# Kernel optimization log

Hardware: AMD Instinct MI355X
Metric: run time of the kernel (lower is better)

## Reference

```python
import jax, jax.numpy as jnp
import numpy as np

N_CELLS = 8192
IN_DIM = 512
HID_DIM = 1024
OUT_DIM = 512
ENG_DIM = 128  # hardcoded MLP width in BenchMind
N_FACTIONS = 8
SYNC = 0.15
DEBATE = 0.15


def setup_inputs() -> dict:
    key = jax.random.key(0)
    ks = iter(jax.random.split(key, 40))

    def rn(shape, s=1.0):
        return jax.random.normal(next(ks), shape, dtype=jnp.float32) * s

    def lin(out_d, in_d):
        s = 1.0 / np.sqrt(in_d)
        return rn((out_d, in_d), s), rn((out_d,), s)

    a_W1, a_b1 = lin(ENG_DIM, IN_DIM + HID_DIM)
    a_W2, a_b2 = lin(OUT_DIM, ENG_DIM)
    g_W1, g_b1 = lin(ENG_DIM, IN_DIM + HID_DIM)
    g_W2, g_b2 = lin(OUT_DIM, ENG_DIM)
    gru_Wih, gru_bih = lin(3 * HID_DIM, OUT_DIM + 1)
    gru_Whh, gru_bhh = lin(3 * HID_DIM, HID_DIM)
    proj_W, proj_b = lin(HID_DIM, 2 * HID_DIM)
    head_W, head_b = lin(IN_DIM, OUT_DIM)

    psi = rn((N_CELLS, HID_DIM), 0.1)
    psi = psi / (jnp.linalg.norm(psi, axis=-1, keepdims=True) + 1e-8)
    rho_diag = psi ** 2
    rho_offdiag = rn((N_CELLS, HID_DIM), 0.1)
    hiddens = rn((N_CELLS, HID_DIM), 0.1)
    noise_diag = rn((N_CELLS, HID_DIM))
    noise_off = rn((N_CELLS, HID_DIM))
    x = rn((1, IN_DIM))
    gamma = jnp.float32(0.1)

    return dict(x=x, rho_diag=rho_diag, rho_offdiag=rho_offdiag, hiddens=hiddens,
                gamma=gamma, proj_W=proj_W, proj_b=proj_b,
                a_W1=a_W1, a_b1=a_b1, a_W2=a_W2, a_b2=a_b2,
                g_W1=g_W1, g_b1=g_b1, g_W2=g_W2, g_b2=g_b2,
                gru_Wih=gru_Wih, gru_bih=gru_bih, gru_Whh=gru_Whh, gru_bhh=gru_bhh,
                head_W=head_W, head_b=head_b,
                noise_diag=noise_diag, noise_off=noise_off, step=10)


def _process(x, rho_diag, rho_offdiag, hiddens, gamma, proj_W, proj_b,
             a_W1, a_b1, a_W2, a_b2, g_W1, g_b1, g_W2, g_b2,
             gru_Wih, gru_bih, gru_Whh, gru_bhh, head_W, head_b,
             noise_diag, noise_off, step):
    n = hiddens.shape[0]
    # --- decohere() --- (gamma used via .item() in torch -> non-differentiable)
    g = jax.lax.stop_gradient(jax.nn.sigmoid(gamma))
    rho_off = rho_offdiag * (1.0 - g)
    rho_d = jax.nn.softmax(rho_diag + noise_diag * g * 0.1, axis=-1)
    feat = jnp.concatenate([rho_d, jnp.abs(rho_off)], axis=-1)        # [N, 2H]
    inj = feat @ proj_W.T + proj_b                                     # [N, H]
    h = hiddens + jax.lax.stop_gradient(inj) * 0.1

    # --- batched BenchMind over all cells (torch loops cells one-by-one) ---
    xb = jnp.broadcast_to(x, (n, x.shape[-1]))
    comb = jnp.concatenate([xb, h], axis=-1)                           # [N, I+H]
    a = jax.nn.relu(comb @ a_W1.T + a_b1) @ a_W2.T + a_b2              # [N, O]
    gg = jax.nn.relu(comb @ g_W1.T + g_b1) @ g_W2.T + g_b2             # [N, O]
    out = a - gg
    tension = jnp.mean(out ** 2, axis=-1, keepdims=True)               # [N, 1]

    # GRUCell (torch gate order: r, z, n); inputs are detached in torch
    mem_in = jax.lax.stop_gradient(jnp.concatenate([out, tension], axis=-1))
    gi = mem_in @ gru_Wih.T + gru_bih                                  # [N, 3H]
    gh = h @ gru_Whh.T + gru_bhh                                       # [N, 3H]
    i_r, i_z, i_n = jnp.split(gi, 3, axis=-1)
    h_r, h_z, h_n = jnp.split(gh, 3, axis=-1)
    r = jax.nn.sigmoid(i_r + h_r)
    z = jax.nn.sigmoid(i_z + h_z)
    nn_ = jnp.tanh(i_n + r * h_n)
    new_h = jax.lax.stop_gradient((1.0 - z) * nn_ + z * h)             # .detach() in torch

    # --- faction_sync_debate ---
    nf = min(N_FACTIONS, n // 2)
    fs = n // nf
    hb = new_h[: nf * fs].reshape(nf, fs, -1)
    hb = (1.0 - SYNC) * hb + SYNC * hb.mean(axis=1, keepdims=True)
    if step > 5:
        glob = hb.mean(axis=1).mean(axis=0)                            # [H]
        dc = max(1, fs // 4)
        hb = hb.at[:, :dc].set((1.0 - DEBATE) * hb[:, :dc] + DEBATE * glob)
    new_h = hb.reshape(nf * fs, -1)

    # --- tension-weighted mixture (weights built from .item()s -> no grad) ---
    w = jax.nn.softmax(jax.lax.stop_gradient(tension[:, 0]))           # [N]
    combined = (w[:, None] * out).sum(axis=0, keepdims=True)           # [1, O]
    pred = combined @ head_W.T + head_b                                # [1, I]
    return pred, new_h


def reference(x, rho_diag, rho_offdiag, hiddens, gamma, proj_W, proj_b,
              a_W1, a_b1, a_W2, a_b2, g_W1, g_b1, g_W2, g_b2,
              gru_Wih, gru_bih, gru_Whh, gru_bhh, head_W, head_b,
              noise_diag, noise_off, step):
    return _process(x, rho_diag, rho_offdiag, hiddens, gamma, proj_W, proj_b,
                    a_W1, a_b1, a_W2, a_b2, g_W1, g_b1, g_W2, g_b2,
                    gru_Wih, gru_bih, gru_Whh, gru_bhh, head_W, head_b,
                    noise_diag, noise_off, step)
```

## Files before the change

kernel.cpp:

```cpp
#include <hip/hip_runtime.h>
#include <math.h>

#define NC 8192
#define ID 512
#define HD 1024
#define OD 512
#define ED 128
#define NF 8
#define FS (NC/NF)
#define DC (FS/4)

typedef __bf16 bf16x8 __attribute__((ext_vector_type(8)));
typedef float  f32x4  __attribute__((ext_vector_type(4)));

__device__ __forceinline__ float sigmf(float x){ return 1.0f/(1.0f+__expf(-x)); }

__device__ __forceinline__ unsigned short f2bf(float f){
  union { float f; unsigned u; } v; v.f = f;
  unsigned r = v.u + 0x7FFFu + ((v.u >> 16) & 1u);
  return (unsigned short)(r >> 16);
}
__device__ __forceinline__ float bf2f(unsigned short b){
  union { unsigned u; float f; } v; v.u = ((unsigned)b) << 16;
  return v.f;
}
__device__ __forceinline__ void gload16(const void* g, void* l){
  __builtin_amdgcn_global_load_lds(
      (const __attribute__((address_space(1))) unsigned int*)g,
      (__attribute__((address_space(3))) unsigned int*)l, 16, 0, 0);
}

__global__ __launch_bounds__(256) void k_conv(
    const float* __restrict__ src, unsigned short* __restrict__ dst,
    int rows, int cols, int sld, int sofs, int dld, float scale)
{
  int i = blockIdx.x*256 + threadIdx.x;
  int total = rows*cols/4;
  if (i >= total) return;
  int r = (i*4)/cols, c = (i*4)%cols;
  const float* s = src + (size_t)r*sld + sofs + c;
  unsigned long long pack = 0;
  for (int q=0;q<4;q++)
    pack |= (unsigned long long)f2bf(s[q]*scale) << (16*q);
  *reinterpret_cast<unsigned long long*>(&dst[(size_t)r*dld + c]) = pack;
}

__global__ __launch_bounds__(256) void k_convgru(
    const float* __restrict__ Wih, const float* __restrict__ Whh,
    unsigned short* __restrict__ dst)
{
  int i = blockIdx.x*256 + threadIdx.x;
  const int total = 3*1024*1536/4;
  if (i >= total) return;
  int row = (i*4)/1536, c = (i*4)%1536;
  unsigned long long pack = 0;
  if (c < 512){
    const float* s = Wih + (size_t)row*(OD+1) + c;
    for (int q=0;q<4;q++) pack |= (unsigned long long)f2bf(s[q]) << (16*q);
  } else {
    const float* s = Whh + (size_t)row*HD + (c-512);
    for (int q=0;q<4;q++) pack |= (unsigned long long)f2bf(s[q]) << (16*q);
  }
  *reinterpret_cast<unsigned long long*>(&dst[(size_t)row*1536 + c]) = pack;
}

__global__ __launch_bounds__(256) void k_feat(
    const float* __restrict__ rho_diag, const float* __restrict__ noise_diag,
    const float* __restrict__ rho_off,  const float* __restrict__ gamma,
    unsigned short* __restrict__ featb)
{
  int row = blockIdx.x;
  int t = threadIdx.x;
  float g = 1.0f/(1.0f+__expf(-gamma[0]));
  const float* rd = rho_diag  + (size_t)row*HD;
  const float* nd = noise_diag+ (size_t)row*HD;
  const float* ro = rho_off   + (size_t)row*HD;
  unsigned short* f0 = featb + (size_t)row*(2*HD);

  float v[4];
  float mx = -1e30f;
  for (int i=0;i<4;i++){ int j=t+i*256; v[i] = rd[j] + nd[j]*g*0.1f; mx = fmaxf(mx, v[i]); }
  __shared__ float red[256];
  red[t]=mx; __syncthreads();
  for(int s=128;s>0;s>>=1){ if(t<s) red[t]=fmaxf(red[t],red[t+s]); __syncthreads(); }
  mx = red[0]; __syncthreads();
  float sm=0.0f;
  for(int i=0;i<4;i++){ v[i]=__expf(v[i]-mx); sm+=v[i]; }
  red[t]=sm; __syncthreads();
  for(int s=128;s>0;s>>=1){ if(t<s) red[t]+=red[t+s]; __syncthreads(); }
  float inv = 1.0f/red[0];
  float om_g = 1.0f - g;
  for(int i=0;i<4;i++){
    int j=t+i*256;
    f0[j]     = f2bf(v[i]*inv);
    f0[HD+j]  = f2bf(fabsf(ro[j])*om_g);
  }
}

template<int MODE>
__global__ __launch_bounds__(256) void k_mgemm(
    const unsigned short* __restrict__ A, int lda,
    const unsigned short* __restrict__ W,
    int K, int N,
    float* __restrict__ Cf, int ldcf,
    unsigned short* __restrict__ Cb, int ldcb,
    const float* __restrict__ e0, const float* __restrict__ e1)
{
  __shared__ __attribute__((aligned(16))) unsigned short Asb[128*32];
  __shared__ __attribute__((aligned(16))) unsigned short Bsb[128*32];
  const int t = threadIdx.x;
  const int lane = t & 63, wid = t >> 6;
  const int wr = wid >> 1, wc = wid & 1;

  const int nwg = gridDim.x*gridDim.y;
  const int bid = blockIdx.y*gridDim.x + blockIdx.x;
  const int swz = (bid & 7)*(nwg >> 3) + (bid >> 3);
  const int m0 = (swz / gridDim.x) * 128, n0 = (swz % gridDim.x) * 128;

  const int srow = lane >> 2;
  const int skch = (lane & 3) * 8;
  const int fr = lane & 15, fk = (lane >> 4) * 8;

  f32x4 acc[4][4] = {};
  for (int k0 = 0; k0 < K; k0 += 32) {
    for (int q = 0; q < 2; ++q) {
      int r = wid*32 + q*16 + srow;
      gload16(A + (size_t)(m0 + r)*lda + k0 + skch, &Asb[(wid*32 + q*16)*32]);
      gload16(W + (size_t)(n0 + r)*K   + k0 + skch, &Bsb[(wid*32 + q*16)*32]);
    }
    __syncthreads();
    bf16x8 af[4], bfr[4];
    for (int i = 0; i < 4; ++i)
      af[i]  = *reinterpret_cast<const bf16x8*>(&Asb[(wr*64 + i*16 + fr)*32 + fk]);
    for (int j = 0; j < 4; ++j)
      bfr[j] = *reinterpret_cast<const bf16x8*>(&Bsb[(wc*64 + j*16 + fr)*32 + fk]);
    for (int i = 0; i < 4; ++i)
      for (int j = 0; j < 4; ++j)
        acc[i][j] = __builtin_amdgcn_mfma_f32_16x16x32_bf16(af[i], bfr[j], acc[i][j], 0, 0, 0);
    __syncthreads();
  }
  const int cr = (lane >> 4) * 4;
  const int cc = lane & 15;
  for (int i = 0; i < 4; ++i){
    for (int j = 0; j < 4; ++j){
      for (int r = 0; r < 4; ++r){
        int m = m0 + wr*64 + i*16 + cr + r;
        int n = n0 + wc*64 + j*16 + cc;
        float v = acc[i][j][r];
        if (MODE == 0)      v = e0[(size_t)m*N + n] + 0.1f*(v + e1[n]);
        else if (MODE == 1) v = fmaxf(v + e0[n], 0.0f);
        else if (MODE == 2) v = v + e0[n];
        if (MODE == 2) Cf[(size_t)m*ldcf + n] = v;
        Cb[(size_t)m*ldcb + n] = f2bf(v);
      }
    }
  }
}

__global__ __launch_bounds__(256) void k_gru_mega(
    const unsigned short* __restrict__ Acat,
    const unsigned short* __restrict__ Wg,
    const float* __restrict__ bih, const float* __restrict__ bhh,
    const float* __restrict__ tens, const float* __restrict__ wlast,
    float* __restrict__ newh)
{
  __shared__ __attribute__((aligned(16))) unsigned short As[64*32];
  __shared__ __attribute__((aligned(16))) unsigned short Rs[64*32];
  __shared__ __attribute__((aligned(16))) unsigned short Zs[64*32];
  __shared__ __attribute__((aligned(16))) unsigned short Ns[64*32];
  const int t = threadIdx.x;
  const int lane = t & 63, wid = t >> 6;
  const int wr = wid >> 1, wc = wid & 1;

  const int nwg = gridDim.x*gridDim.y;
  const int bid = blockIdx.y*gridDim.x + blockIdx.x;
  const int swz = (bid & 7)*(nwg >> 3) + (bid >> 3);
  const int m0 = (swz >> 4) * 64, n0 = (swz & 15) * 64;

  const int srow = lane >> 2;
  const int skch = (lane & 3) * 8;
  const int fr = lane & 15, fk = (lane >> 4) * 8;

  const unsigned short* sbase;
  unsigned short* lbase;
  if      (wid == 0){ sbase = Acat + (size_t)m0*1536;              lbase = As; }
  else if (wid == 1){ sbase = Wg   + (size_t)n0*1536;              lbase = Rs; }
  else if (wid == 2){ sbase = Wg + (size_t)(HD + n0)*1536;         lbase = Zs; }
  else              { sbase = Wg + (size_t)(2*HD + n0)*1536;       lbase = Ns; }

  f32x4 acc_r[2][2] = {}, acc_z[2][2] = {}, acc_na[2][2] = {}, acc_nb[2][2] = {};

  for (int k0 = 0; k0 < 1536; k0 += 32) {
    for (int q = 0; q < 4; ++q)
      gload16(sbase + (size_t)(q*16 + srow)*1536 + k0 + skch, &lbase[(q*16)*32]);
    __syncthreads();
    bf16x8 af[2], br[2], bz[2], bn[2];
    for (int i = 0; i < 2; ++i)
      af[i] = *reinterpret_cast<const bf16x8*>(&As[(wr*32 + i*16 + fr)*32 + fk]);
    for (int j = 0; j < 2; ++j){
      br[j] = *reinterpret_cast<const bf16x8*>(&Rs[(wc*32 + j*16 + fr)*32 + fk]);
      bz[j] = *reinterpret_cast<const bf16x8*>(&Zs[(wc*32 + j*16 + fr)*32 + fk]);
      bn[j] = *reinterpret_cast<const bf16x8*>(&Ns[(wc*32 + j*16 + fr)*32 + fk]);
    }
    if (k0 < 512){
      for (int i = 0; i < 2; ++i)
        for (int j = 0; j < 2; ++j){
          acc_r [i][j] = __builtin_amdgcn_mfma_f32_16x16x32_bf16(af[i], br[j], acc_r [i][j], 0,0,0);
          acc_z [i][j] = __builtin_amdgcn_mfma_f32_16x16x32_bf16(af[i], bz[j], acc_z [i][j], 0,0,0);
          acc_na[i][j] = __builtin_amdgcn_mfma_f32_16x16x32_bf16(af[i], bn[j], acc_na[i][j], 0,0,0);
        }
    } else {
      for (int i = 0; i < 2; ++i)
        for (int j = 0; j < 2; ++j){
          acc_r [i][j] = __builtin_amdgcn_mfma_f32_16x16x32_bf16(af[i], br[j], acc_r [i][j], 0,0,0);
          acc_z [i][j] = __builtin_amdgcn_mfma_f32_16x16x32_bf16(af[i], bz[j], acc_z [i][j], 0,0,0);
          acc_nb[i][j] = __builtin_amdgcn_mfma_f32_16x16x32_bf16(af[i], bn[j], acc_nb[i][j], 0,0,0);
        }
    }
    __syncthreads();
  }

  const int cr = (lane >> 4) * 4;
  const int cc = lane & 15;
  for (int i = 0; i < 2; ++i){
    for (int r = 0; r < 4; ++r){
      int m = m0 + wr*32 + i*16 + cr + r;
      float tm = tens[m];
      for (int j = 0; j < 2; ++j){
        int n = n0 + wc*32 + j*16 + cc;
        float sr  = acc_r [i][j][r] + bih[n]      + tm*wlast[n]      + bhh[n];
        float sz  = acc_z [i][j][r] + bih[HD+n]   + tm*wlast[HD+n]   + bhh[HD+n];
        float sni = acc_na[i][j][r] + bih[2*HD+n] + tm*wlast[2*HD+n];
        float snh = acc_nb[i][j][r] + bhh[2*HD+n];
        float rg = sigmf(sr);
        float zg = sigmf(sz);
        float nn = tanhf(sni + rg*snh);
        float hv = bf2f(Acat[(size_t)m*1536 + 512 + n]);
        newh[(size_t)m*HD + n] = (1.0f - zg)*nn + zg*hv;
      }
    }
  }
}

__global__ __launch_bounds__(128) void k_xpart(
    const float* __restrict__ x,
    const float* __restrict__ aW1, const float* __restrict__ ab1,
    const float* __restrict__ gW1, const float* __restrict__ gb1,
    const float* __restrict__ Wih,
    const float* __restrict__ ab2, const float* __restrict__ gb2,
    float* __restrict__ xcat, float* __restrict__ wlast, float* __restrict__ b2diff)
{
  int t = threadIdx.x;
  if (blockIdx.x == 2){
    for (int n=t; n<3*HD; n+=128) wlast[n] = Wih[(size_t)n*(OD+1) + OD];
    for (int n=t; n<OD;   n+=128) b2diff[n] = ab2[n] - gb2[n];
    return;
  }
  const float* W = blockIdx.x ? gW1 : aW1;
  const float* b = blockIdx.x ? gb1 : ab1;
  float s = b[t];
  const float* wr = W + (size_t)t*(ID+HD);
  for (int k=0;k<ID;k++) s += x[k]*wr[k];
  xcat[blockIdx.x*ED + t] = s;
}

__global__ __launch_bounds__(256) void k_tension(
    const float* __restrict__ outp, float* __restrict__ tens)
{
  int m = blockIdx.x, t = threadIdx.x;
  float s = 0.0f;
  for (int j=t;j<OD;j+=256){ float v = outp[(size_t)m*OD + j]; s += v*v; }
  __shared__ float red[256];
  red[t]=s; __syncthreads();
  for(int k=128;k>0;k>>=1){ if(t<k) red[t]+=red[t+k]; __syncthreads(); }
  if (t==0) tens[m] = red[0] * (1.0f/OD);
}

__global__ __launch_bounds__(256) void k_fmean(
    const float* __restrict__ newh, float* __restrict__ fmean)
{
  int f = blockIdx.x;
  int j = blockIdx.y*256 + threadIdx.x;
  const float* base = newh + (size_t)f*FS*HD + j;
  float s = 0.0f;
  for (int c=0;c<FS;c++) s += base[(size_t)c*HD];
  fmean[f*HD + j] = s * (1.0f/FS);
}

__global__ __launch_bounds__(256) void k_sync(
    float* __restrict__ newh, const float* __restrict__ fmean,
    const int* __restrict__ step)
{
  size_t idx = (size_t)blockIdx.x*256 + threadIdx.x;
  int cell = (int)(idx / HD);
  int j    = (int)(idx % HD);
  int f = cell / FS, c = cell % FS;
  float v = newh[idx];
  v = 0.85f*v + 0.15f*fmean[f*HD + j];
  if (step[0] > 5 && c < DC){
    float glob = 0.0f;
    for (int ff=0; ff<NF; ff++) glob += fmean[ff*HD + j];
    glob *= (1.0f/NF);
    v = 0.85f*v + 0.15f*glob;
  }
  newh[idx] = v;
}

__global__ __launch_bounds__(1024) void k_wstats(
    const float* __restrict__ tens, float* __restrict__ stats)
{
  int t = threadIdx.x;
  float mx = -1e30f;
  for (int i=t;i<NC;i+=1024) mx = fmaxf(mx, tens[i]);
  __shared__ float red[1024];
  red[t]=mx; __syncthreads();
  for(int s=512;s>0;s>>=1){ if(t<s) red[t]=fmaxf(red[t],red[t+s]); __syncthreads(); }
  mx = red[0]; __syncthreads();
  float sm=0.0f;
  for (int i=t;i<NC;i+=1024) sm += __expf(tens[i]-mx);
  red[t]=sm; __syncthreads();
  for(int s=512;s>0;s>>=1){ if(t<s) red[t]+=red[t+s]; __syncthreads(); }
  if (t==0){ stats[0]=mx; stats[1]=red[0]; }
}

__global__ __launch_bounds__(256) void k_wnorm(
    const float* __restrict__ tens, const float* __restrict__ stats,
    float* __restrict__ w)
{
  int m = blockIdx.x*256 + threadIdx.x;
  w[m] = __expf(tens[m]-stats[0]) * (1.0f/stats[1]);
}

__global__ __launch_bounds__(256) void k_comb1(
    const float* __restrict__ outp, const float* __restrict__ w,
    float* __restrict__ partial)
{
  int b = blockIdx.x, t = threadIdx.x;
  float a0 = 0.0f, a1 = 0.0f;
  for (int m = 0; m < 128; ++m){
    int row = b*128 + m;
    float wm = w[row];
    const float* r = outp + (size_t)row*OD;
    a0 += wm * r[t];
    a1 += wm * r[t+256];
  }
  partial[(size_t)b*OD + t]       = a0;
  partial[(size_t)b*OD + t + 256] = a1;
}

__global__ __launch_bounds__(256) void k_comb2(
    const float* __restrict__ partial, float* __restrict__ comb)
{
  int n = blockIdx.x*256 + threadIdx.x;
  float s = 0.0f;
  for (int b = 0; b < 64; ++b) s += partial[(size_t)b*OD + n];
  comb[n] = s;
}

__global__ __launch_bounds__(128) void k_pred(
    const float* __restrict__ comb, const float* __restrict__ headW,
    const float* __restrict__ headb, float* __restrict__ pred)
{
  int i = blockIdx.x, t = threadIdx.x;
  float s = 0.0f;
  const float* wr = headW + (size_t)i*OD;
  for (int k=t;k<OD;k+=128) s += comb[k]*wr[k];
  __shared__ float red[128];
  red[t]=s; __syncthreads();
  for (int sx=64;sx>0;sx>>=1){ if(t<sx) red[t]+=red[t+sx]; __syncthreads(); }
  if (t==0) pred[i] = red[0] + headb[i];
}

extern "C" void kernel_launch(void* const* d_in, const int* in_sizes, int n_in,
                              void* d_out, int out_size, void* d_ws, size_t ws_size,
                              hipStream_t stream)
{
  const float* x        = (const float*)d_in[0];
  const float* rho_diag = (const float*)d_in[1];
  const float* rho_off  = (const float*)d_in[2];
  const float* hiddens  = (const float*)d_in[3];
  const float* gamma    = (const float*)d_in[4];
  const float* proj_W   = (const float*)d_in[5];
  const float* proj_b   = (const float*)d_in[6];
  const float* a_W1     = (const float*)d_in[7];
  const float* a_b1     = (const float*)d_in[8];
  const float* a_W2     = (const float*)d_in[9];
  const float* a_b2     = (const float*)d_in[10];
  const float* g_W1     = (const float*)d_in[11];
  const float* g_b1     = (const float*)d_in[12];
  const float* g_W2     = (const float*)d_in[13];
  const float* g_b2     = (const float*)d_in[14];
  const float* gru_Wih  = (const float*)d_in[15];
  const float* gru_bih  = (const float*)d_in[16];
  const float* gru_Whh  = (const float*)d_in[17];
  const float* gru_bhh  = (const float*)d_in[18];
  const float* head_W   = (const float*)d_in[19];
  const float* head_b   = (const float*)d_in[20];
  const float* noise_d  = (const float*)d_in[21];
  const int*   step     = (const int*)d_in[23];

  float* pred = (float*)d_out;
  float* newh = (float*)d_out + ID;

  char* ws = (char*)d_ws;
  const size_t MB = 1024*1024;
  unsigned short* Acat   = (unsigned short*)(ws + 0);
  unsigned short* featb  = (unsigned short*)(ws + 24*MB);
  float*          outp_f = (float*)(ws + 56*MB);
  unsigned short* eag    = (unsigned short*)(ws + 72*MB);
  unsigned short* wProj  = (unsigned short*)(ws + 76*MB);
  unsigned short* wGru   = (unsigned short*)(ws + 80*MB);
  unsigned short* wEng   = (unsigned short*)(ws + 89*MB);
  unsigned short* wW2    = (unsigned short*)(ws + 89*MB + 512*1024);
  char* sm = ws + 90*MB;
  float* tens    = (float*)(sm + 0);
  float* xcat    = (float*)(sm + 64*1024);
  float* wlast   = (float*)(sm + 128*1024);
  float* b2diff  = (float*)(sm + 160*1024);
  float* fmean   = (float*)(sm + 192*1024);
  float* stats   = (float*)(sm + 256*1024);
  float* wts     = (float*)(sm + 320*1024);
  float* partial = (float*)(sm + 384*1024);
  float* comb    = (float*)(sm + 576*1024);

  dim3 blk(256);
  #define CONVGRID(n) dim3(((n)/4 + 255)/256)

  k_conv<<<CONVGRID(1024*2048), blk, 0, stream>>>(proj_W, wProj, 1024, 2048, 2048, 0, 2048, 1.0f);
  k_convgru<<<dim3(3*1024*1536/4/256), blk, 0, stream>>>(gru_Wih, gru_Whh, wGru);
  k_conv<<<CONVGRID(128*1024), blk, 0, stream>>>(a_W1, wEng,            128, 1024, ID+HD, ID, 1024, 1.0f);
  k_conv<<<CONVGRID(128*1024), blk, 0, stream>>>(g_W1, wEng + 128*1024, 128, 1024, ID+HD, ID, 1024, 1.0f);
  k_conv<<<CONVGRID(512*128),  blk, 0, stream>>>(a_W2, wW2,       512, 128, 128, 0, 256,  1.0f);
  k_conv<<<CONVGRID(512*128),  blk, 0, stream>>>(g_W2, wW2 + 128, 512, 128, 128, 0, 256, -1.0f);

  k_feat<<<dim3(NC), blk, 0, stream>>>(rho_diag, noise_d, rho_off, gamma, featb);
  k_xpart<<<dim3(3), dim3(128), 0, stream>>>(x, a_W1, a_b1, g_W1, g_b1, gru_Wih,
                                             a_b2, g_b2, xcat, wlast, b2diff);

  k_mgemm<0><<<dim3(HD/128, NC/128), blk, 0, stream>>>(
      featb, 2*HD, wProj, 2*HD, HD, nullptr, 0, Acat + 512, 1536, hiddens, proj_b);
  k_mgemm<1><<<dim3(256/128, NC/128), blk, 0, stream>>>(
      Acat + 512, 1536, wEng, HD, 256, nullptr, 0, eag, 256, xcat, nullptr);
  k_mgemm<2><<<dim3(OD/128, NC/128), blk, 0, stream>>>(
      eag, 256, wW2, 256, OD, outp_f, OD, Acat, 1536, b2diff, nullptr);
  k_tension<<<dim3(NC), blk, 0, stream>>>(outp_f, tens);
  k_gru_mega<<<dim3(HD/64, NC/64), blk, 0, stream>>>(
      Acat, wGru, gru_bih, gru_bhh, tens, wlast, newh);
  k_fmean<<<dim3(NF, HD/256), blk, 0, stream>>>(newh, fmean);
  k_sync<<<dim3((NC*HD)/256), blk, 0, stream>>>(newh, fmean, step);
  k_wstats<<<dim3(1), dim3(1024), 0, stream>>>(tens, stats);
  k_wnorm<<<dim3(NC/256), blk, 0, stream>>>(tens, stats, wts);
  k_comb1<<<dim3(64), blk, 0, stream>>>(outp_f, wts, partial);
  k_comb2<<<dim3(2), blk, 0, stream>>>(partial, comb);
  k_pred<<<dim3(ID), dim3(128), 0, stream>>>(comb, head_W, head_b, pred);
}
```

Before: 602.8 us.

## Double-buffer LDS tiles in GEMM and GRU kernels, reorder block mapping

Both the generic MFMA GEMM and the fused GRU kernel now use two LDS buffers per operand, so the next K-slice is loaded while the current one is consumed, which removes one barrier per iteration. The workgroup-to-tile mapping is also changed to walk along M first within each N column, so neighbouring blocks reuse the same weight tile in cache. LDS use doubles, which may lower occupancy. Correctness relies on the gload16 async copy having completed by the single barrier at the end of each iteration.

```diff
diff --git a/kernel.cpp b/kernel.cpp
--- a/kernel.cpp
+++ b/kernel.cpp
@@ -106,8 +106,8 @@
     unsigned short* __restrict__ Cb, int ldcb,
     const float* __restrict__ e0, const float* __restrict__ e1)
 {
-  __shared__ __attribute__((aligned(16))) unsigned short Asb[128*32];
-  __shared__ __attribute__((aligned(16))) unsigned short Bsb[128*32];
+  __shared__ __attribute__((aligned(16))) unsigned short Asb[2][128*32];
+  __shared__ __attribute__((aligned(16))) unsigned short Bsb[2][128*32];
   const int t = threadIdx.x;
   const int lane = t & 63, wid = t >> 6;
   const int wr = wid >> 1, wc = wid & 1;
@@ -115,30 +115,45 @@
   const int nwg = gridDim.x*gridDim.y;
   const int bid = blockIdx.y*gridDim.x + blockIdx.x;
   const int swz = (bid & 7)*(nwg >> 3) + (bid >> 3);
-  const int m0 = (swz / gridDim.x) * 128, n0 = (swz % gridDim.x) * 128;
+  const int n0 = (swz / gridDim.y) * 128, m0 = (swz % gridDim.y) * 128;
 
   const int srow = lane >> 2;
   const int skch = (lane & 3) * 8;
   const int fr = lane & 15, fk = (lane >> 4) * 8;
 
+  const int nk = K >> 5;
   f32x4 acc[4][4] = {};
-  for (int k0 = 0; k0 < K; k0 += 32) {
+
+  {
     for (int q = 0; q < 2; ++q) {
       int r = wid*32 + q*16 + srow;
-      gload16(A + (size_t)(m0 + r)*lda + k0 + skch, &Asb[(wid*32 + q*16)*32]);
-      gload16(W + (size_t)(n0 + r)*K   + k0 + skch, &Bsb[(wid*32 + q*16)*32]);
-    }
-    __syncthreads();
+      gload16(A + (size_t)(m0 + r)*lda + skch, &Asb[0][(wid*32 + q*16)*32]);
+      gload16(W + (size_t)(n0 + r)*K   + skch, &Bsb[0][(wid*32 + q*16)*32]);
+    }
+  }
+  __syncthreads();
+
+  for (int kk = 0; kk < nk; ++kk) {
+    const int buf = kk & 1;
+    if (kk + 1 < nk) {
+      const int k0 = (kk + 1) << 5;
+      for (int q = 0; q < 2; ++q) {
+        int r = wid*32 + q*16 + srow;
+        gload16(A + (size_t)(m0 + r)*lda + k0 + skch, &Asb[buf^1][(wid*32 + q*16)*32]);
+        gload16(W + (size_t)(n0 + r)*K   + k0 + skch, &Bsb[buf^1][(wid*32 + q*16)*32]);
+      }
+    }
     bf16x8 af[4], bfr[4];
     for (int i = 0; i < 4; ++i)
-      af[i]  = *reinterpret_cast<const bf16x8*>(&Asb[(wr*64 + i*16 + fr)*32 + fk]);
+      af[i]  = *reinterpret_cast<const bf16x8*>(&Asb[buf][(wr*64 + i*16 + fr)*32 + fk]);
     for (int j = 0; j < 4; ++j)
-      bfr[j] = *reinterpret_cast<const bf16x8*>(&Bsb[(wc*64 + j*16 + fr)*32 + fk]);
+      bfr[j] = *reinterpret_cast<const bf16x8*>(&Bsb[buf][(wc*64 + j*16 + fr)*32 + fk]);
     for (int i = 0; i < 4; ++i)
       for (int j = 0; j < 4; ++j)
         acc[i][j] = __builtin_amdgcn_mfma_f32_16x16x32_bf16(af[i], bfr[j], acc[i][j], 0, 0, 0);
     __syncthreads();
   }
+
   const int cr = (lane >> 4) * 4;
   const int cc = lane & 15;
   for (int i = 0; i < 4; ++i){
@@ -164,10 +179,10 @@
     const float* __restrict__ tens, const float* __restrict__ wlast,
     float* __restrict__ newh)
 {
-  __shared__ __attribute__((aligned(16))) unsigned short As[64*32];
-  __shared__ __attribute__((aligned(16))) unsigned short Rs[64*32];
-  __shared__ __attribute__((aligned(16))) unsigned short Zs[64*32];
-  __shared__ __attribute__((aligned(16))) unsigned short Ns[64*32];
+  __shared__ __attribute__((aligned(16))) unsigned short As[2][64*32];
+  __shared__ __attribute__((aligned(16))) unsigned short Rs[2][64*32];
+  __shared__ __attribute__((aligned(16))) unsigned short Zs[2][64*32];
+  __shared__ __attribute__((aligned(16))) unsigned short Ns[2][64*32];
   const int t = threadIdx.x;
   const int lane = t & 63, wid = t >> 6;
   const int wr = wid >> 1, wc = wid & 1;
@@ -175,42 +190,58 @@
   const int nwg = gridDim.x*gridDim.y;
   const int bid = blockIdx.y*gridDim.x + blockIdx.x;
   const int swz = (bid & 7)*(nwg >> 3) + (bid >> 3);
-  const int m0 = (swz >> 4) * 64, n0 = (swz & 15) * 64;
+  const int n0 = (swz / gridDim.y) * 64, m0 = (swz % gridDim.y) * 64;
 
   const int srow = lane >> 2;
   const int skch = (lane & 3) * 8;
   const int fr = lane & 15, fk = (lane >> 4) * 8;
 
   const unsigned short* sbase;
-  unsigned short* lbase;
-  if      (wid == 0){ sbase = Acat + (size_t)m0*1536;              lbase = As; }
-  else if (wid == 1){ sbase = Wg   + (size_t)n0*1536;              lbase = Rs; }
-  else if (wid == 2){ sbase = Wg + (size_t)(HD + n0)*1536;         lbase = Zs; }
-  else              { sbase = Wg + (size_t)(2*HD + n0)*1536;       lbase = Ns; }
+  unsigned short* lb0; unsigned short* lb1;
+  if      (wid == 0){ sbase = Acat + (size_t)m0*1536;          lb0 = As[0]; lb1 = As[1]; }
+  else if (wid == 1){ sbase = Wg   + (size_t)n0*1536;          lb0 = Rs[0]; lb1 = Rs[1]; }
+  else if (wid == 2){ sbase = Wg + (size_t)(HD   + n0)*1536;   lb0 = Zs[0]; lb1 = Zs[1]; }
+  else              { sbase = Wg + (size_t)(2*HD + n0)*1536;   lb0 = Ns[0]; lb1 = Ns[1]; }
 
   f32x4 acc_r[2][2] = {}, acc_z[2][2] = {}, acc_na[2][2] = {}, acc_nb[2][2] = {};
 
-  for (int k0 = 0; k0 < 1536; k0 += 32) {
-    for (int q = 0; q < 4; ++q)
-      gload16(sbase + (size_t)(q*16 + srow)*1536 + k0 + skch, &lbase[(q*16)*32]);
-    __syncthreads();
+  #pragma unroll
+  for (int q = 0; q < 4; ++q)
+    gload16(sbase + (size_t)(q*16 + srow)*1536 + skch, &lb0[(q*16)*32]);
+  __syncthreads();
+
+  for (int kk = 0; kk < 48; ++kk) {
+    const int buf = kk & 1;
+    if (kk < 47) {
+      const int k0 = (kk + 1) << 5;
+      unsigned short* lb = buf ? lb0 : lb1;
+      #pragma unroll
+      for (int q = 0; q < 4; ++q)
+        gload16(sbase + (size_t)(q*16 + srow)*1536 + k0 + skch, &lb[(q*16)*32]);
+    }
     bf16x8 af[2], br[2], bz[2], bn[2];
+    #pragma unroll
     for (int i = 0; i < 2; ++i)
-      af[i] = *reinterpret_cast<const bf16x8*>(&As[(wr*32 + i*16 + fr)*32 + fk]);
+      af[i] = *reinterpret_cast<const bf16x8*>(&As[buf][(wr*32 + i*16 + fr)*32 + fk]);
+    #pragma unroll
     for (int j = 0; j < 2; ++j){
-      br[j] = *reinterpret_cast<const bf16x8*>(&Rs[(wc*32 + j*16 + fr)*32 + fk]);
-      bz[j] = *reinterpret_cast<const bf16x8*>(&Zs[(wc*32 + j*16 + fr)*32 + fk]);
-      bn[j] = *reinterpret_cast<const bf16x8*>(&Ns[(wc*32 + j*16 + fr)*32 + fk]);
-    }
-    if (k0 < 512){
+      br[j] = *reinterpret_cast<const bf16x8*>(&Rs[buf][(wc*32 + j*16 + fr)*32 + fk]);
+      bz[j] = *reinterpret_cast<const bf16x8*>(&Zs[buf][(wc*32 + j*16 + fr)*32 + fk]);
+      bn[j] = *reinterpret_cast<const bf16x8*>(&Ns[buf][(wc*32 + j*16 + fr)*32 + fk]);
+    }
+    if (kk < 16){
+      #pragma unroll
       for (int i = 0; i < 2; ++i)
+        #pragma unroll
         for (int j = 0; j < 2; ++j){
           acc_r [i][j] = __builtin_amdgcn_mfma_f32_16x16x32_bf16(af[i], br[j], acc_r [i][j], 0,0,0);
           acc_z [i][j] = __builtin_amdgcn_mfma_f32_16x16x32_bf16(af[i], bz[j], acc_z [i][j], 0,0,0);
           acc_na[i][j] = __builtin_amdgcn_mfma_f32_16x16x32_bf16(af[i], bn[j], acc_na[i][j], 0,0,0);
         }
     } else {
+      #pragma unroll
       for (int i = 0; i < 2; ++i)
+        #pragma unroll
         for (int j = 0; j < 2; ++j){
           acc_r [i][j] = __builtin_amdgcn_mfma_f32_16x16x32_bf16(af[i], br[j], acc_r [i][j], 0,0,0);
           acc_z [i][j] = __builtin_amdgcn_mfma_f32_16x16x32_bf16(af[i], bz[j], acc_z [i][j], 0,0,0);
```

New measurement: 591.7 us. Within noise of the previous version (-1.8%).

## Triple-buffer GEMM LDS loads and merge weight-prep kernels into one launch

Applied to the files above, without the earlier changes.

Both MFMA GEMM kernels now use three LDS buffers, issuing global-to-LDS loads two k-steps ahead and waiting with explicit vmcnt counts before each barrier. This replaces the load-sync-compute-sync pattern so memory latency can overlap with the MFMA work. The mgemm tile order is changed to walk M-major within N columns. The six weight conversion kernels and the x-projection kernel are merged into a single k_prep launch to cut launch overhead. The cost is three times the LDS per block, which may lower occupancy.

```diff
diff --git a/kernel.cpp b/kernel.cpp
--- a/kernel.cpp
+++ b/kernel.cpp
@@ -29,39 +29,62 @@
       (const __attribute__((address_space(1))) unsigned int*)g,
       (__attribute__((address_space(3))) unsigned int*)l, 16, 0, 0);
 }
-
-__global__ __launch_bounds__(256) void k_conv(
-    const float* __restrict__ src, unsigned short* __restrict__ dst,
-    int rows, int cols, int sld, int sofs, int dld, float scale)
-{
-  int i = blockIdx.x*256 + threadIdx.x;
-  int total = rows*cols/4;
-  if (i >= total) return;
-  int r = (i*4)/cols, c = (i*4)%cols;
-  const float* s = src + (size_t)r*sld + sofs + c;
-  unsigned long long pack = 0;
-  for (int q=0;q<4;q++)
-    pack |= (unsigned long long)f2bf(s[q]*scale) << (16*q);
-  *reinterpret_cast<unsigned long long*>(&dst[(size_t)r*dld + c]) = pack;
-}
-
-__global__ __launch_bounds__(256) void k_convgru(
-    const float* __restrict__ Wih, const float* __restrict__ Whh,
-    unsigned short* __restrict__ dst)
-{
-  int i = blockIdx.x*256 + threadIdx.x;
-  const int total = 3*1024*1536/4;
-  if (i >= total) return;
-  int row = (i*4)/1536, c = (i*4)%1536;
-  unsigned long long pack = 0;
-  if (c < 512){
-    const float* s = Wih + (size_t)row*(OD+1) + c;
-    for (int q=0;q<4;q++) pack |= (unsigned long long)f2bf(s[q]) << (16*q);
+__device__ __forceinline__ void pack4(const float* s, unsigned short* d, float sc){
+  unsigned long long p = 0;
+  for (int q=0;q<4;q++) p |= (unsigned long long)f2bf(s[q]*sc) << (16*q);
+  *reinterpret_cast<unsigned long long*>(d) = p;
+}
+
+#define WAIT_VM4()  asm volatile("s_waitcnt vmcnt(4)" ::: "memory")
+#define WAIT_VM0()  asm volatile("s_waitcnt vmcnt(0)" ::: "memory")
+#define BARRIER()   do { __builtin_amdgcn_s_barrier(); asm volatile("" ::: "memory"); } while(0)
+
+__global__ __launch_bounds__(256) void k_prep(
+    const float* __restrict__ proj_W, const float* __restrict__ Wih,
+    const float* __restrict__ Whh,
+    const float* __restrict__ aW1, const float* __restrict__ gW1,
+    const float* __restrict__ aW2, const float* __restrict__ gW2,
+    const float* __restrict__ x,
+    const float* __restrict__ ab1, const float* __restrict__ gb1,
+    const float* __restrict__ ab2, const float* __restrict__ gb2,
+    unsigned short* __restrict__ wProj, unsigned short* __restrict__ wGru,
+    unsigned short* __restrict__ wEng,  unsigned short* __restrict__ wW2,
+    float* __restrict__ xcat, float* __restrict__ wlast,
+    float* __restrict__ b2diff)
+{
+  int b = blockIdx.x, t = threadIdx.x;
+  if (b < 2048){
+    int i = b*256 + t; int r = (i*4)>>11, c = (i*4)&2047;
+    pack4(proj_W + (size_t)r*2048 + c, wProj + (size_t)r*2048 + c, 1.0f);
+  } else if (b < 6656){
+    int i = (b-2048)*256 + t; int row = (i*4)/1536, c = (i*4)%1536;
+    const float* s = (c < 512) ? (Wih + (size_t)row*(OD+1) + c)
+                               : (Whh + (size_t)row*HD + (c-512));
+    pack4(s, wGru + (size_t)row*1536 + c, 1.0f);
+  } else if (b < 6784){
+    int i = (b-6656)*256 + t; int r = (i*4)>>10, c = (i*4)&1023;
+    pack4(aW1 + (size_t)r*(ID+HD) + ID + c, wEng + (size_t)r*1024 + c, 1.0f);
+  } else if (b < 6912){
+    int i = (b-6784)*256 + t; int r = (i*4)>>10, c = (i*4)&1023;
+    pack4(gW1 + (size_t)r*(ID+HD) + ID + c, wEng + 128*1024 + (size_t)r*1024 + c, 1.0f);
+  } else if (b < 6976){
+    int i = (b-6912)*256 + t; int r = (i*4)>>7, c = (i*4)&127;
+    pack4(aW2 + (size_t)r*128 + c, wW2 + (size_t)r*256 + c, 1.0f);
+  } else if (b < 7040){
+    int i = (b-6976)*256 + t; int r = (i*4)>>7, c = (i*4)&127;
+    pack4(gW2 + (size_t)r*128 + c, wW2 + (size_t)r*256 + 128 + c, -1.0f);
+  } else if (b == 7040){
+    const float* W  = (t < 128) ? aW1 : gW1;
+    const float* bb = (t < 128) ? ab1 : gb1;
+    int n = t & 127;
+    float s = bb[n];
+    const float* wr = W + (size_t)n*(ID+HD);
+    for (int k=0;k<ID;k++) s += x[k]*wr[k];
+    xcat[t] = s;
   } else {
-    const float* s = Whh + (size_t)row*HD + (c-512);
-    for (int q=0;q<4;q++) pack |= (unsigned long long)f2bf(s[q]) << (16*q);
-  }
-  *reinterpret_cast<unsigned long long*>(&dst[(size_t)row*1536 + c]) = pack;
+    for (int n=t; n<3*HD; n+=256) wlast[n] = Wih[(size_t)n*(OD+1) + OD];
+    for (int n=t; n<OD;   n+=256) b2diff[n] = ab2[n] - gb2[n];
+  }
 }
 
 __global__ __launch_bounds__(256) void k_feat(
@@ -106,8 +129,8 @@
     unsigned short* __restrict__ Cb, int ldcb,
     const float* __restrict__ e0, const float* __restrict__ e1)
 {
-  __shared__ __attribute__((aligned(16))) unsigned short Asb[128*32];
-  __shared__ __attribute__((aligned(16))) unsigned short Bsb[128*32];
+  __shared__ __attribute__((aligned(16))) unsigned short Asb[3][128*32];
+  __shared__ __attribute__((aligned(16))) unsigned short Bsb[3][128*32];
   const int t = threadIdx.x;
   const int lane = t & 63, wid = t >> 6;
   const int wr = wid >> 1, wc = wid & 1;
@@ -115,30 +138,51 @@
   const int nwg = gridDim.x*gridDim.y;
   const int bid = blockIdx.y*gridDim.x + blockIdx.x;
   const int swz = (bid & 7)*(nwg >> 3) + (bid >> 3);
-  const int m0 = (swz / gridDim.x) * 128, n0 = (swz % gridDim.x) * 128;
+  const int n0 = (swz / gridDim.y) * 128, m0 = (swz % gridDim.y) * 128;
 
   const int srow = lane >> 2;
   const int skch = (lane & 3) * 8;
   const int fr = lane & 15, fk = (lane >> 4) * 8;
 
+  const int nk = K >> 5;
   f32x4 acc[4][4] = {};
-  for (int k0 = 0; k0 < K; k0 += 32) {
+
+  auto STAGE = [&](int kc, int bf){
+    const int k0 = kc << 5;
     for (int q = 0; q < 2; ++q) {
       int r = wid*32 + q*16 + srow;
-      gload16(A + (size_t)(m0 + r)*lda + k0 + skch, &Asb[(wid*32 + q*16)*32]);
-      gload16(W + (size_t)(n0 + r)*K   + k0 + skch, &Bsb[(wid*32 + q*16)*32]);
-    }
-    __syncthreads();
+      gload16(A + (size_t)(m0 + r)*lda + k0 + skch, &Asb[bf][(wid*32 + q*16)*32]);
+      gload16(W + (size_t)(n0 + r)*K   + k0 + skch, &Bsb[bf][(wid*32 + q*16)*32]);
+    }
+  };
+
+  STAGE(0, 0);
+  if (nk > 1) { STAGE(1, 1); WAIT_VM4(); } else { WAIT_VM0(); }
+  BARRIER();
+
+  for (int kk = 0; kk < nk; ++kk) {
+    const int buf = kk % 3;
+    if (kk + 2 < nk) STAGE(kk + 2, (kk + 2) % 3);
+    const unsigned short* Ab = &Asb[buf][0];
+    const unsigned short* Bb = &Bsb[buf][0];
     bf16x8 af[4], bfr[4];
+    #pragma unroll
     for (int i = 0; i < 4; ++i)
-      af[i]  = *reinterpret_cast<const bf16x8*>(&Asb[(wr*64 + i*16 + fr)*32 + fk]);
+      af[i]  = *reinterpret_cast<const bf16x8*>(&Ab[(wr*64 + i*16 + fr)*32 + fk]);
+    #pragma unroll
     for (int j = 0; j < 4; ++j)
-      bfr[j] = *reinterpret_cast<const bf16x8*>(&Bsb[(wc*64 + j*16 + fr)*32 + fk]);
+      bfr[j] = *reinterpret_cast<const bf16x8*>(&Bb[(wc*64 + j*16 + fr)*32 + fk]);
+    #pragma unroll
     for (int i = 0; i < 4; ++i)
+      #pragma unroll
       for (int j = 0; j < 4; ++j)
         acc[i][j] = __builtin_amdgcn_mfma_f32_16x16x32_bf16(af[i], bfr[j], acc[i][j], 0, 0, 0);
-    __syncthreads();
-  }
+    if (kk + 1 < nk) {
+      if (kk + 2 < nk) WAIT_VM4(); else WAIT_VM0();
+      BARRIER();
+    }
+  }
+
   const int cr = (lane >> 4) * 4;
   const int cc = lane & 15;
   for (int i = 0; i < 4; ++i){
@@ -164,10 +208,10 @@
     const float* __restrict__ tens, const float* __restrict__ wlast,
     float* __restrict__ newh)
 {
-  __shared__ __attribute__((aligned(16))) unsigned short As[64*32];
-  __shared__ __attribute__((aligned(16))) unsigned short Rs[64*32];
-  __shared__ __attribute__((aligned(16))) unsigned short Zs[64*32];
-  __shared__ __attribute__((aligned(16))) unsigned short Ns[64*32];
+  __shared__ __attribute__((aligned(16))) unsigned short As[3][64*32];
+  __shared__ __attribute__((aligned(16))) unsigned short Rs[3][64*32];
+  __shared__ __attribute__((aligned(16))) unsigned short Zs[3][64*32];
+  __shared__ __attribute__((aligned(16))) unsigned short Ns[3][64*32];
   const int t = threadIdx.x;
   const int lane = t & 63, wid = t >> 6;
   const int wr = wid >> 1, wc = wid & 1;
@@ -182,42 +226,68 @@
   const int fr = lane & 15, fk = (lane >> 4) * 8;
 
   const unsigned short* sbase;
-  unsigned short* lbase;
-  if      (wid == 0){ sbase = Acat + (size_t)m0*1536;              lbase = As; }
-  else if (wid == 1){ sbase = Wg   + (size_t)n0*1536;              lbase = Rs; }
-  else if (wid == 2){ sbase = Wg + (size_t)(HD + n0)*1536;         lbase = Zs; }
-  else              { sbase = Wg + (size_t)(2*HD + n0)*1536;       lbase = Ns; }
+  unsigned short* lb;
+  if      (wid == 0){ sbase = Acat + (size_t)m0*1536;          lb = &As[0][0]; }
+  else if (wid == 1){ sbase = Wg   + (size_t)n0*1536;          lb = &Rs[0][0]; }
+  else if (wid == 2){ sbase = Wg + (size_t)(HD   + n0)*1536;   lb = &Zs[0][0]; }
+  else              { sbase = Wg + (size_t)(2*HD + n0)*1536;   lb = &Ns[0][0]; }
 
   f32x4 acc_r[2][2] = {}, acc_z[2][2] = {}, acc_na[2][2] = {}, acc_nb[2][2] = {};
 
-  for (int k0 = 0; k0 < 1536; k0 += 32) {
+  auto STAGE = [&](int kc, int bf){
+    const int k0 = kc << 5;
+    #pragma unroll
     for (int q = 0; q < 4; ++q)
-      gload16(sbase + (size_t)(q*16 + srow)*1536 + k0 + skch, &lbase[(q*16)*32]);
-    __syncthreads();
+      gload16(sbase + (size_t)(q*16 + srow)*1536 + k0 + skch,
+              lb + bf*(64*32) + (q*16)*32);
+  };
+
+  STAGE(0, 0);
+  STAGE(1, 1);
+  WAIT_VM4();
+  BARRIER();
+
+  const int nk = 48;
+  for (int kk = 0; kk < nk; ++kk) {
+    const int buf = kk % 3;
+    if (kk + 2 < nk) STAGE(kk + 2, (kk + 2) % 3);
+    const unsigned short* Ab = &As[0][0] + buf*(64*32);
+    const unsigned short* Rb = &Rs[0][0] + buf*(64*32);
+    const unsigned short* Zb = &Zs[0][0] + buf*(64*32);
+    const unsigned short* Nb = &Ns[0][0] + buf*(64*32);
     bf16x8 af[2], br[2], bz[2], bn[2];
+    #pragma unroll
     for (int i = 0; i < 2; ++i)
-      af[i] = *reinterpret_cast<const bf16x8*>(&As[(wr*32 + i*16 + fr)*32 + fk]);
+      af[i] = *reinterpret_cast<const bf16x8*>(&Ab[(wr*32 + i*16 + fr)*32 + fk]);
+    #pragma unroll
     for (int j = 0; j < 2; ++j){
-      br[j] = *reinterpret_cast<const bf16x8*>(&Rs[(wc*32 + j*16 + fr)*32 + fk]);
-      bz[j] = *reinterpret_cast<const bf16x8*>(&Zs[(wc*32 + j*16 + fr)*32 + fk]);
-      bn[j] = *reinterpret_cast<const bf16x8*>(&Ns[(wc*32 + j*16 + fr)*32 + fk]);
-    }
-    if (k0 < 512){
+      br[j] = *reinterpret_cast<const bf16x8*>(&Rb[(wc*32 + j*16 + fr)*32 + fk]);
+      bz[j] = *reinterpret_cast<const bf16x8*>(&Zb[(wc*32 + j*16 + fr)*32 + fk]);
+      bn[j] = *reinterpret_cast<const bf16x8*>(&Nb[(wc*32 + j*16 + fr)*32 + fk]);
+    }
+    if (kk < 16){
+      #pragma unroll
       for (int i = 0; i < 2; ++i)
+        #pragma unroll
         for (int j = 0; j < 2; ++j){
           acc_r [i][j] = __builtin_amdgcn_mfma_f32_16x16x32_bf16(af[i], br[j], acc_r [i][j], 0,0,0);
           acc_z [i][j] = __builtin_amdgcn_mfma_f32_16x16x32_bf16(af[i], bz[j], acc_z [i][j], 0,0,0);
           acc_na[i][j] = __builtin_amdgcn_mfma_f32_16x16x32_bf16(af[i], bn[j], acc_na[i][j], 0,0,0);
         }
     } else {
+      #pragma unroll
       for (int i = 0; i < 2; ++i)
+        #pragma unroll
         for (int j = 0; j < 2; ++j){
           acc_r [i][j] = __builtin_amdgcn_mfma_f32_16x16x32_bf16(af[i], br[j], acc_r [i][j], 0,0,0);
           acc_z [i][j] = __builtin_amdgcn_mfma_f32_16x16x32_bf16(af[i], bz[j], acc_z [i][j], 0,0,0);
           acc_nb[i][j] = __builtin_amdgcn_mfma_f32_16x16x32_bf16(af[i], bn[j], acc_nb[i][j], 0,0,0);
         }
     }
-    __syncthreads();
+    if (kk + 1 < nk) {
+      if (kk + 2 < nk) WAIT_VM4(); else WAIT_VM0();
+      BARRIER();
+    }
   }
 
   const int cr = (lane >> 4) * 4;
@@ -240,28 +310,6 @@
       }
     }
   }
-}
-
-__global__ __launch_bounds__(128) void k_xpart(
-    const float* __restrict__ x,
-    const float* __restrict__ aW1, const float* __restrict__ ab1,
-    const float* __restrict__ gW1, const float* __restrict__ gb1,
-    const float* __restrict__ Wih,
-    const float* __restrict__ ab2, const float* __restrict__ gb2,
-    float* __restrict__ xcat, float* __restrict__ wlast, float* __restrict__ b2diff)
-{
-  int t = threadIdx.x;
-  if (blockIdx.x == 2){
-    for (int n=t; n<3*HD; n+=128) wlast[n] = Wih[(size_t)n*(OD+1) + OD];
-    for (int n=t; n<OD;   n+=128) b2diff[n] = ab2[n] - gb2[n];
-    return;
-  }
-  const float* W = blockIdx.x ? gW1 : aW1;
-  const float* b = blockIdx.x ? gb1 : ab1;
-  float s = b[t];
-  const float* wr = W + (size_t)t*(ID+HD);
-  for (int k=0;k<ID;k++) s += x[k]*wr[k];
-  xcat[blockIdx.x*ED + t] = s;
 }
 
 __global__ __launch_bounds__(256) void k_tension(
@@ -424,18 +472,11 @@
   float* comb    = (float*)(sm + 576*1024);
 
   dim3 blk(256);
-  #define CONVGRID(n) dim3(((n)/4 + 255)/256)
-
-  k_conv<<<CONVGRID(1024*2048), blk, 0, stream>>>(proj_W, wProj, 1024, 2048, 2048, 0, 2048, 1.0f);
-  k_convgru<<<dim3(3*1024*1536/4/256), blk, 0, stream>>>(gru_Wih, gru_Whh, wGru);
-  k_conv<<<CONVGRID(128*1024), blk, 0, stream>>>(a_W1, wEng,            128, 1024, ID+HD, ID, 1024, 1.0f);
-  k_conv<<<CONVGRID(128*1024), blk, 0, stream>>>(g_W1, wEng + 128*1024, 128, 1024, ID+HD, ID, 1024, 1.0f);
-  k_conv<<<CONVGRID(512*128),  blk, 0, stream>>>(a_W2, wW2,       512, 128, 128, 0, 256,  1.0f);
-  k_conv<<<CONVGRID(512*128),  blk, 0, stream>>>(g_W2, wW2 + 128, 512, 128, 128, 0, 256, -1.0f);
-
+
+  k_prep<<<dim3(7042), blk, 0, stream>>>(
+      proj_W, gru_Wih, gru_Whh, a_W1, g_W1, a_W2, g_W2, x,
+      a_b1, g_b1, a_b2, g_b2, wProj, wGru, wEng, wW2, xcat, wlast, b2diff);
   k_feat<<<dim3(NC), blk, 0, stream>>>(rho_diag, noise_d, rho_off, gamma, featb);
-  k_xpart<<<dim3(3), dim3(128), 0, stream>>>(x, a_W1, a_b1, g_W1, g_b1, gru_Wih,
-                                             a_b2, g_b2, xcat, wlast, b2diff);
 
   k_mgemm<0><<<dim3(HD/128, NC/128), blk, 0, stream>>>(
       featb, 2*HD, wProj, 2*HD, HD, nullptr, 0, Acat + 512, 1536, hiddens, proj_b);
```

After: 579.1 us. -3.9%, faster.
